# Performance work log

Measured on AMD Instinct MI355X. Metric: run time of the kernel, lower is better.

The kernel has to match this reference:

```python
import jax, jax.numpy as jnp
import numpy as np

N = 100000   # nodes
E = 1600000  # directed edges (avg degree 16)
D = 128      # num_feature == hidden_channels


def setup_inputs() -> dict:
    key = jax.random.key(0)
    ks = jax.random.split(key, 8)
    s = 1.0 / np.sqrt(D)
    x = jax.random.normal(ks[0], (N, D), jnp.float32)
    edge_index = jax.random.randint(ks[1], (2, E), 0, N, dtype=jnp.int32)
    W1 = jax.random.normal(ks[2], (D, D), jnp.float32) * s
    W2 = jax.random.normal(ks[3], (D, D), jnp.float32) * s
    W3 = jax.random.normal(ks[4], (D, D), jnp.float32) * s
    b1 = jnp.zeros((D,), jnp.float32)
    b2 = jnp.zeros((D,), jnp.float32)
    b3 = jnp.zeros((D,), jnp.float32)
    return {"x": x, "edge_index": edge_index, "W1": W1, "b1": b1,
            "W2": W2, "b2": b2, "W3": W3, "b3": b3}


def reference(x, edge_index, W1, b1, W2, b2, W3, b3):
    # GCNConv with added self-loops and symmetric normalization:
    #   out = D^{-1/2} (A + I) D^{-1/2} (x W) + b
    loops = jnp.arange(N, dtype=edge_index.dtype)
    src = jnp.concatenate([edge_index[0], loops])  # [E+N]
    dst = jnp.concatenate([edge_index[1], loops])
    deg = jax.ops.segment_sum(jnp.ones_like(dst, x.dtype), dst, num_segments=N)
    dinv = jax.lax.rsqrt(deg)                      # deg >= 1 (self-loops)
    norm = dinv[src] * dinv[dst]                   # [E+N]

    def conv(h, W, b):
        h = h @ W                                   # [N, D] dense GEMM
        msg = h[src] * norm[:, None]                # gather + scale [E+N, D]
        return jax.ops.segment_sum(msg, dst, num_segments=N) + b

    # dropout is identity in eval mode
    h = jax.nn.relu(conv(x, W1, b1))
    h = jax.nn.relu(conv(h, W2, b2))
    return conv(h, W3, b3)
```

## Files before the change

kernel.cpp:

```cpp
#include <hip/hip_runtime.h>
#include <hip/hip_fp16.h>

#define DFEAT 128
#define BNODES 256
#define BSHIFT 8
#define B1CHUNK 4096
#define SLABC 8192
#define TPB_TILES 2
#define TPB1 2

typedef _Float16 f16x8 __attribute__((ext_vector_type(8)));
typedef _Float16 f16x4 __attribute__((ext_vector_type(4)));
typedef float f32x4 __attribute__((ext_vector_type(4)));


__global__ __launch_bounds__(256) void packW_k(const float* __restrict__ W0, const float* __restrict__ W1,
                                               const float* __restrict__ W2,
                                               const float* __restrict__ b0, const float* __restrict__ b1,
                                               const float* __restrict__ b2,
                                               _Float16* __restrict__ wpk, float* __restrict__ bp,
                                               int* __restrict__ gcnt) {
    int idx = blockIdx.x * 256 + threadIdx.x;
    int layer = idx >> 14;
    int e = idx & 16383;
    int k = e >> 7;
    int nn = e & 127;
    const float* W = (layer == 0) ? W0 : ((layer == 1) ? W1 : W2);
    int ksrc = (layer == 0) ? k : (((k & 7) << 4) | (k >> 3));
    float v = W[ksrc * DFEAT + nn];
    int kc = k >> 5, quad = (k >> 3) & 3, j = k & 7;
    int ct = nn >> 4;
    int pos = ((ct * 4 + kc) * 64 + quad * 16 + (nn & 15)) * 8 + j;
    wpk[(size_t)layer * 16384 + pos] = (_Float16)v;
    if (idx < 384) {
        int l = idx >> 7, p = idx & 127;
        int c = ((p & 7) << 4) | (p >> 3);
        const float* bb = (l == 0) ? b0 : ((l == 1) ? b1 : b2);
        bp[l * 128 + p] = bb[c];
    }
    if (idx < 512) gcnt[idx] = 0;
}

__device__ inline f16x8 ldA8(const float* p) {
    float4 a = *(const float4*)p;
    float4 b = *(const float4*)(p + 4);
    return f16x8{(_Float16)a.x, (_Float16)a.y, (_Float16)a.z, (_Float16)a.w,
                 (_Float16)b.x, (_Float16)b.y, (_Float16)b.z, (_Float16)b.w};
}
__device__ inline f16x8 ldA8(const __half* p) { return *(const f16x8*)p; }
__device__ inline f16x8 zero8() {
    return f16x8{(_Float16)0.f, (_Float16)0.f, (_Float16)0.f, (_Float16)0.f,
                 (_Float16)0.f, (_Float16)0.f, (_Float16)0.f, (_Float16)0.f};
}

struct BinSh {
    int cnt[512];
    int off[512];
    int gbase[512];
    int sd[256];
    unsigned int buf[B1CHUNK];
    unsigned short bid[B1CHUNK];
};
struct G1Sh {
    _Float16 wl[16384];
};

__global__ __launch_bounds__(256) void binGemm1_k(const int* __restrict__ src, const int* __restrict__ dst,
                                                  int* __restrict__ gcnt, unsigned int* __restrict__ slab,
                                                  int E, int nbuck, int nbin,
                                                  const float* __restrict__ A, const _Float16* __restrict__ wfrag,
                                                  __half* __restrict__ C, int n, int ntiles) {
    __shared__ __align__(16) char smem[32768];
    int t = threadIdx.x;
    if (blockIdx.x >= nbin) {
        _Float16* wl = ((G1Sh*)smem)->wl;
        const int wv_ = t >> 6;
        const int lane = t & 63;
        const int m = lane & 15;
        const int q = lane >> 4;
        for (int c = t; c < 2048; c += 256)
            *(f16x8*)&wl[c * 8] = *(const f16x8*)&wfrag[c * 8];
        __syncthreads();
        int t0 = (blockIdx.x - nbin) * TPB1;
        int tend = t0 + TPB1;
        if (tend > ntiles) tend = ntiles;
        for (int tile = t0; tile < tend; ++tile) {
            int row0 = tile * 64;
            int ga = row0 + wv_ * 16 + m;
            f16x8 af[4];
            if (ga < n) {
#pragma unroll
                for (int kc = 0; kc < 4; ++kc)
                    af[kc] = ldA8(&A[(size_t)ga * DFEAT + kc * 32 + q * 8]);
            } else {
#pragma unroll
                for (int kc = 0; kc < 4; ++kc) af[kc] = zero8();
            }
            f32x4 acc[8];
#pragma unroll
            for (int ct = 0; ct < 8; ++ct) acc[ct] = (f32x4){0.f, 0.f, 0.f, 0.f};
#pragma unroll
            for (int ct = 0; ct < 8; ++ct) {
#pragma unroll
                for (int kc = 0; kc < 4; ++kc) {
                    f16x8 bf = *(f16x8*)&wl[((ct * 4 + kc) * 64 + lane) * 8];
                    acc[ct] = __builtin_amdgcn_mfma_f32_16x16x32_f16(af[kc], bf, acc[ct], 0, 0, 0);
                }
            }
            const int rbase = row0 + wv_ * 16 + q * 4;
#pragma unroll
            for (int r = 0; r < 4; ++r) {
                int gr = rbase + r;
                if (gr < n) {
                    f16x8 o;
#pragma unroll
                    for (int ct = 0; ct < 8; ++ct) o[ct] = (_Float16)acc[ct][r];
                    *(f16x8*)&C[(size_t)gr * DFEAT + m * 8] = o;
                }
            }
        }
        return;
    }
    BinSh* B = (BinSh*)smem;
    int base = blockIdx.x * B1CHUNK;
    int nloc = E - base;
    if (nloc > B1CHUNK) nloc = B1CHUNK;
    B->cnt[t] = 0;
    B->cnt[t + 256] = 0;
    __syncthreads();
    int k = t;
    for (; k + 768 < nloc; k += 1024) {
        int d0 = dst[base + k], d1 = dst[base + k + 256], d2 = dst[base + k + 512], d3 = dst[base + k + 768];
        atomicAdd(&B->cnt[d0 >> BSHIFT], 1);
        atomicAdd(&B->cnt[d1 >> BSHIFT], 1);
        atomicAdd(&B->cnt[d2 >> BSHIFT], 1);
        atomicAdd(&B->cnt[d3 >> BSHIFT], 1);
    }
    for (; k < nloc; k += 256) atomicAdd(&B->cnt[dst[base + k] >> BSHIFT], 1);
    __syncthreads();
    int v0 = B->cnt[2 * t], v1 = B->cnt[2 * t + 1];
    int tsum = v0 + v1;
    B->sd[t] = tsum;
    __syncthreads();
    for (int o = 1; o < 256; o <<= 1) {
        int x = (t >= o) ? B->sd[t - o] : 0;
        __syncthreads();
        B->sd[t] += x;
        __syncthreads();
    }
    int texcl = B->sd[t] - tsum;
    B->off[2 * t] = texcl;
    B->off[2 * t + 1] = texcl + v0;
    if (2 * t < nbuck && v0 > 0) B->gbase[2 * t] = atomicAdd(&gcnt[2 * t], v0);
    if (2 * t + 1 < nbuck && v1 > 0) B->gbase[2 * t + 1] = atomicAdd(&gcnt[2 * t + 1], v1);
    __syncthreads();
    k = t;
    for (; k + 768 < nloc; k += 1024) {
        int d0 = dst[base + k], d1 = dst[base + k + 256], d2 = dst[base + k + 512], d3 = dst[base + k + 768];
        int s0 = src[base + k], s1 = src[base + k + 256], s2 = src[base + k + 512], s3 = src[base + k + 768];
        int b0_ = d0 >> BSHIFT, b1_ = d1 >> BSHIFT, b2_ = d2 >> BSHIFT, b3_ = d3 >> BSHIFT;
        int r0 = atomicAdd(&B->off[b0_], 1); B->buf[r0] = ((unsigned)s0 << BSHIFT) | (unsigned)(d0 & (BNODES - 1)); B->bid[r0] = (unsigned short)b0_;
        int r1 = atomicAdd(&B->off[b1_], 1); B->buf[r1] = ((unsigned)s1 << BSHIFT) | (unsigned)(d1 & (BNODES - 1)); B->bid[r1] = (unsigned short)b1_;
        int r2 = atomicAdd(&B->off[b2_], 1); B->buf[r2] = ((unsigned)s2 << BSHIFT) | (unsigned)(d2 & (BNODES - 1)); B->bid[r2] = (unsigned short)b2_;
        int r3 = atomicAdd(&B->off[b3_], 1); B->buf[r3] = ((unsigned)s3 << BSHIFT) | (unsigned)(d3 & (BNODES - 1)); B->bid[r3] = (unsigned short)b3_;
    }
    for (; k < nloc; k += 256) {
        int d = dst[base + k];
        int s = src[base + k];
        int b = d >> BSHIFT;
        int r = atomicAdd(&B->off[b], 1);
        B->buf[r] = ((unsigned)s << BSHIFT) | (unsigned)(d & (BNODES - 1));
        B->bid[r] = (unsigned short)b;
    }
    __syncthreads();
    k = t;
    for (; k + 768 < nloc; k += 1024) {
#pragma unroll
        for (int u = 0; u < 4; ++u) {
            int kk = k + u * 256;
            int b = B->bid[kk];
            int o0 = B->off[b] - B->cnt[b];
            int pos = B->gbase[b] + (kk - o0);
            if (pos < SLABC) slab[(size_t)b * SLABC + pos] = B->buf[kk];
        }
    }
    for (; k < nloc; k += 256) {
        int b = B->bid[k];
        int o0 = B->off[b] - B->cnt[b];
        int pos = B->gbase[b] + (k - o0);
        if (pos < SLABC) slab[(size_t)b * SLABC + pos] = B->buf[k];
    }
}

__global__ __launch_bounds__(256) void bucketAB_k(const unsigned int* __restrict__ slab,
                                                  const int* __restrict__ gcnt,
                                                  int* __restrict__ rp, float* __restrict__ dinv,
                                                  int* __restrict__ cols, int N, int nbuck) {
    __shared__ int cnt[256];
    __shared__ int cur[256];
    __shared__ int psum[256];
    __shared__ int outb[SLABC];
    int t = threadIdx.x;
    int b = blockIdx.x;
    int n0 = b << BSHIFT;
    int nn = N - n0;
    if (nn > BNODES) nn = BNODES;
    int ne_raw = gcnt[b];
    int ne = ne_raw > SLABC ? SLABC : ne_raw;
    const unsigned int* sl = slab + (size_t)b * SLABC;
    int part = 0;
    for (int i = t; i < b; i += 256) part += gcnt[i];
    psum[t] = part;
    cnt[t] = 0;
    __syncthreads();
    for (int o = 128; o > 0; o >>= 1) {
        if (t < o) psum[t] += psum[t + o];
        __syncthreads();
    }
    int base = psum[0];
    int k = t;
    for (; k + 768 < ne; k += 1024) {
        unsigned a0 = sl[k], a1 = sl[k + 256], a2 = sl[k + 512], a3 = sl[k + 768];
        atomicAdd(&cnt[a0 & (BNODES - 1)], 1);
        atomicAdd(&cnt[a1 & (BNODES - 1)], 1);
        atomicAdd(&cnt[a2 & (BNODES - 1)], 1);
        atomicAdd(&cnt[a3 & (BNODES - 1)], 1);
    }
    for (; k < ne; k += 256) atomicAdd(&cnt[sl[k] & (BNODES - 1)], 1);
    __syncthreads();
    int deg = cnt[t];
    for (int o = 1; o < 256; o <<= 1) {
        int x = (t >= o) ? cnt[t - o] : 0;
        __syncthreads();
        cnt[t] += x;
        __syncthreads();
    }
    int excl = cnt[t] - deg;
    if (t < nn) {
        rp[n0 + t] = base + excl;
        dinv[n0 + t] = rsqrtf((float)(deg + 1));
    }
    if (b == nbuck - 1 && t == 0) rp[N] = base + ne_raw;
    cur[t] = excl;
    __syncthreads();
    k = t;
    for (; k + 768 < ne; k += 1024) {
        unsigned a0 = sl[k], a1 = sl[k + 256], a2 = sl[k + 512], a3 = sl[k + 768];
        int p0 = atomicAdd(&cur[a0 & (BNODES - 1)], 1); outb[p0] = (int)(a0 >> BSHIFT);
        int p1 = atomicAdd(&cur[a1 & (BNODES - 1)], 1); outb[p1] = (int)(a1 >> BSHIFT);
        int p2 = atomicAdd(&cur[a2 & (BNODES - 1)], 1); outb[p2] = (int)(a2 >> BSHIFT);
        int p3 = atomicAdd(&cur[a3 & (BNODES - 1)], 1); outb[p3] = (int)(a3 >> BSHIFT);
    }
    for (; k < ne; k += 256) {
        unsigned a = sl[k];
        int p = atomicAdd(&cur[a & (BNODES - 1)], 1);
        outb[p] = (int)(a >> BSHIFT);
    }
    __syncthreads();
    k = t;
    for (; k + 768 < ne; k += 1024) {
        int o0 = outb[k], o1 = outb[k + 256], o2 = outb[k + 512], o3 = outb[k + 768];
        cols[base + k] = o0;
        cols[base + k + 256] = o1;
        cols[base + k + 512] = o2;
        cols[base + k + 768] = o3;
    }
    for (; k < ne; k += 256) cols[base + k] = outb[k];
}

template <typename TIN>
__global__ __launch_bounds__(256) void gemmP_k(const TIN* __restrict__ A, const _Float16* __restrict__ wfrag,
                                               const float* __restrict__ dinv, __half* __restrict__ C,
                                               int n, int ntiles) {
    __shared__ _Float16 al[8192];
    __shared__ _Float16 wl[16384];
    const int tid = threadIdx.x;
    const int wv_ = tid >> 6;
    const int lane = tid & 63;
    const int t0 = blockIdx.x * TPB_TILES;
    const int chunk = tid & 15;
    const int rsub = tid >> 4;
    const int kcS = chunk >> 2, quadS = chunk & 3;
    const int swzS = (kcS << 1) ^ (quadS & 1);

    for (int c = tid; c < 2048; c += 256)
        *(f16x8*)&wl[c * 8] = *(const f16x8*)&wfrag[c * 8];

    f16x8 pre[4];
    {
        int row0 = t0 * 64;
#pragma unroll
        for (int p = 0; p < 4; ++p) {
            int gr = row0 + p * 16 + rsub;
            pre[p] = (gr < n) ? ldA8(&A[(size_t)gr * DFEAT + chunk * 8]) : zero8();
        }
    }
    for (int tt = 0; tt < TPB_TILES; ++tt) {
        int tile = t0 + tt;
        if (tile >= ntiles) break;
        int row0 = tile * 64;
#pragma unroll
        for (int p = 0; p < 4; ++p) {
            int idx = (p * 4 + kcS) * 64 + quadS * 16 + rsub;
            *(f16x8*)&al[(idx ^ swzS) * 8] = pre[p];
        }
        __syncthreads();
        if (tt + 1 < TPB_TILES && tile + 1 < ntiles) {
            int nrow0 = (tile + 1) * 64;
#pragma unroll
            for (int p = 0; p < 4; ++p) {
                int gr = nrow0 + p * 16 + rsub;
                pre[p] = (gr < n) ? ldA8(&A[(size_t)gr * DFEAT + chunk * 8]) : zero8();
            }
        }
        f16x8 af[4];
        const int swzR = (lane >> 4) & 1;
#pragma unroll
        for (int kc = 0; kc < 4; ++kc) {
            int idx = (wv_ * 4 + kc) * 64 + lane;
            af[kc] = *(f16x8*)&al[(idx ^ (kc << 1) ^ swzR) * 8];
        }
        const int quad = lane >> 4, cb = lane & 15;
        const int rbase = row0 + wv_ * 16 + quad * 4;
        float ds[4];
#pragma unroll
        for (int r = 0; r < 4; ++r) ds[r] = (rbase + r < n) ? dinv[rbase + r] : 0.f;
        f32x4 acc[8];
#pragma unroll
        for (int ct = 0; ct < 8; ++ct) acc[ct] = (f32x4){0.f, 0.f, 0.f, 0.f};
#pragma unroll
        for (int ct = 0; ct < 8; ++ct) {
#pragma unroll
            for (int kc = 0; kc < 4; ++kc) {
                f16x8 bf = *(f16x8*)&wl[((ct * 4 + kc) * 64 + lane) * 8];
                acc[ct] = __builtin_amdgcn_mfma_f32_16x16x32_f16(af[kc], bf, acc[ct], 0, 0, 0);
            }
        }
#pragma unroll
        for (int r = 0; r < 4; ++r) {
            int gr = rbase + r;
            if (gr < n) {
                f16x8 o;
#pragma unroll
                for (int ct = 0; ct < 8; ++ct) o[ct] = (_Float16)(acc[ct][r] * ds[r]);
                *(f16x8*)&C[(size_t)gr * DFEAT + cb * 8] = o;
            }
        }
        __syncthreads();
    }
}


__global__ __launch_bounds__(256) void aggW_k(const __half* __restrict__ T, const float* __restrict__ dinv,
                                              const int* __restrict__ rowptr, const int* __restrict__ cols,
                                              const float* __restrict__ biasp,
                                              __half* __restrict__ out, int n) {
    int wid = (int)((blockIdx.x * (size_t)blockDim.x + threadIdx.x) >> 6);
    int lane = threadIdx.x & 63;
    if (wid >= n) return;
    int fb = lane * 2;
    float di = dinv[wid];
    float2 t0 = __half22float2(*(const __half2*)(T + (size_t)wid * DFEAT + fb));
    float ax = di * t0.x;
    float ay = di * t0.y;
    int s = rowptr[wid], e = rowptr[wid + 1];
    for (int p = s; p < e; ) {
        int take = e - p;
        if (take > 64) take = 64;
        int q = p + lane;
        if (q >= e) q = e - 1;
        int ci = cols[q];
        int j = 0;
        for (; j + 8 <= take; j += 8) {
            int c0 = __builtin_amdgcn_readlane(ci, j + 0);
            int c1 = __builtin_amdgcn_readlane(ci, j + 1);
            int c2 = __builtin_amdgcn_readlane(ci, j + 2);
            int c3 = __builtin_amdgcn_readlane(ci, j + 3);
            int c4 = __builtin_amdgcn_readlane(ci, j + 4);
            int c5 = __builtin_amdgcn_readlane(ci, j + 5);
            int c6 = __builtin_amdgcn_readlane(ci, j + 6);
            int c7 = __builtin_amdgcn_readlane(ci, j + 7);
            float w0 = dinv[c0], w1 = dinv[c1], w2 = dinv[c2], w3 = dinv[c3];
            float w4 = dinv[c4], w5 = dinv[c5], w6 = dinv[c6], w7 = dinv[c7];
            float2 v0 = __half22float2(*(const __half2*)(T + (size_t)c0 * DFEAT + fb));
            float2 v1 = __half22float2(*(const __half2*)(T + (size_t)c1 * DFEAT + fb));
            float2 v2 = __half22float2(*(const __half2*)(T + (size_t)c2 * DFEAT + fb));
            float2 v3 = __half22float2(*(const __half2*)(T + (size_t)c3 * DFEAT + fb));
            float2 v4 = __half22float2(*(const __half2*)(T + (size_t)c4 * DFEAT + fb));
            float2 v5 = __half22float2(*(const __half2*)(T + (size_t)c5 * DFEAT + fb));
            float2 v6 = __half22float2(*(const __half2*)(T + (size_t)c6 * DFEAT + fb));
            float2 v7 = __half22float2(*(const __half2*)(T + (size_t)c7 * DFEAT + fb));
            ax += w0 * v0.x; ay += w0 * v0.y;
            ax += w1 * v1.x; ay += w1 * v1.y;
            ax += w2 * v2.x; ay += w2 * v2.y;
            ax += w3 * v3.x; ay += w3 * v3.y;
            ax += w4 * v4.x; ay += w4 * v4.y;
            ax += w5 * v5.x; ay += w5 * v5.y;
            ax += w6 * v6.x; ay += w6 * v6.y;
            ax += w7 * v7.x; ay += w7 * v7.y;
        }
        for (; j < take; ++j) {
            int c = __builtin_amdgcn_readlane(ci, j);
            float w = dinv[c];
            float2 v = __half22float2(*(const __half2*)(T + (size_t)c * DFEAT + fb));
            ax += w * v.x; ay += w * v.y;
        }
        p += take;
    }
    float ox = fmaxf(di * ax + biasp[fb], 0.f);
    float oy = fmaxf(di * ay + biasp[fb + 1], 0.f);
    *(__half2*)(out + (size_t)wid * DFEAT + fb) = __floats2half2_rn(ox, oy);
}

__device__ inline float2 agg_row(const __half* __restrict__ T, const int* __restrict__ rowptr,
                                 const int* __restrict__ cols, int wid, int lane, int fb) {
    float2 t0 = __half22float2(*(const __half2*)(T + (size_t)wid * DFEAT + fb));
    float ax = t0.x;
    float ay = t0.y;
    int s = rowptr[wid], e = rowptr[wid + 1];
    for (int p = s; p < e; ) {
        int take = e - p;
        if (take > 64) take = 64;
        int q = p + lane;
        if (q >= e) q = e - 1;
        int ci = cols[q];
        int j = 0;
        for (; j + 8 <= take; j += 8) {
            int c0 = __builtin_amdgcn_readlane(ci, j + 0);
            int c1 = __builtin_amdgcn_readlane(ci, j + 1);
            int c2 = __builtin_amdgcn_readlane(ci, j + 2);
            int c3 = __builtin_amdgcn_readlane(ci, j + 3);
            int c4 = __builtin_amdgcn_readlane(ci, j + 4);
            int c5 = __builtin_amdgcn_readlane(ci, j + 5);
            int c6 = __builtin_amdgcn_readlane(ci, j + 6);
            int c7 = __builtin_amdgcn_readlane(ci, j + 7);
            float2 v0 = __half22float2(*(const __half2*)(T + (size_t)c0 * DFEAT + fb));
            float2 v1 = __half22float2(*(const __half2*)(T + (size_t)c1 * DFEAT + fb));
            float2 v2 = __half22float2(*(const __half2*)(T + (size_t)c2 * DFEAT + fb));
            float2 v3 = __half22float2(*(const __half2*)(T + (size_t)c3 * DFEAT + fb));
            float2 v4 = __half22float2(*(const __half2*)(T + (size_t)c4 * DFEAT + fb));
            float2 v5 = __half22float2(*(const __half2*)(T + (size_t)c5 * DFEAT + fb));
            float2 v6 = __half22float2(*(const __half2*)(T + (size_t)c6 * DFEAT + fb));
            float2 v7 = __half22float2(*(const __half2*)(T + (size_t)c7 * DFEAT + fb));
            ax += v0.x; ay += v0.y;
            ax += v1.x; ay += v1.y;
            ax += v2.x; ay += v2.y;
            ax += v3.x; ay += v3.y;
            ax += v4.x; ay += v4.y;
            ax += v5.x; ay += v5.y;
            ax += v6.x; ay += v6.y;
            ax += v7.x; ay += v7.y;
        }
        for (; j < take; ++j) {
            int c = __builtin_amdgcn_readlane(ci, j);
            float2 v = __half22float2(*(const __half2*)(T + (size_t)c * DFEAT + fb));
            ax += v.x; ay += v.y;
        }
        p += take;
    }
    return make_float2(ax, ay);
}

__global__ __launch_bounds__(256) void agg_k(const __half* __restrict__ T, const float* __restrict__ dinv,
                                             const int* __restrict__ rowptr, const int* __restrict__ cols,
                                             const float* __restrict__ biasp,
                                             __half* __restrict__ out, int n) {
    int wid = (int)((blockIdx.x * (size_t)blockDim.x + threadIdx.x) >> 6);
    int lane = threadIdx.x & 63;
    if (wid >= n) return;
    int fb = lane * 2;
    float2 a = agg_row(T, rowptr, cols, wid, lane, fb);
    float dw = dinv[wid];
    float ox = fmaxf(dw * a.x + biasp[fb], 0.f);
    float oy = fmaxf(dw * a.y + biasp[fb + 1], 0.f);
    *(__half2*)(out + (size_t)wid * DFEAT + fb) = __floats2half2_rn(ox, oy);
}

__global__ __launch_bounds__(256) void aggF_k(const __half* __restrict__ T, const float* __restrict__ dinv,
                                              const int* __restrict__ rowptr, const int* __restrict__ cols,
                                              const float* __restrict__ biasp,
                                              float* __restrict__ out, int n) {
    int wid = (int)((blockIdx.x * (size_t)blockDim.x + threadIdx.x) >> 6);
    int lane = threadIdx.x & 63;
    if (wid >= n) return;
    int fb = lane * 2;
    float2 a = agg_row(T, rowptr, cols, wid, lane, fb);
    float dw = dinv[wid];
    float ox = dw * a.x + biasp[fb];
    float oy = dw * a.y + biasp[fb + 1];
    int c0 = ((fb & 7) << 4) | (fb >> 3);
    int c1 = (((fb + 1) & 7) << 4) | ((fb + 1) >> 3);
    out[(size_t)wid * DFEAT + c0] = ox;
    out[(size_t)wid * DFEAT + c1] = oy;
}


extern "C" void kernel_launch(void* const* d_in, const int* in_sizes, int n_in,
                              void* d_out, int out_size, void* d_ws, size_t ws_size,
                              hipStream_t stream) {
    const float* x  = (const float*)d_in[0];
    const int*   ei = (const int*)d_in[1];
    const float* W1 = (const float*)d_in[2];
    const float* b1 = (const float*)d_in[3];
    const float* W2 = (const float*)d_in[4];
    const float* b2 = (const float*)d_in[5];
    const float* W3 = (const float*)d_in[6];
    const float* b3 = (const float*)d_in[7];
    float* out = (float*)d_out;

    const int N = in_sizes[0] / DFEAT;
    const int E = in_sizes[1] / 2;
    const int* srcp = ei;
    const int* dstp = ei + E;

    size_t off = 0;
    auto alloc = [&](size_t bytes) -> void* {
        void* p = (char*)d_ws + off;
        off += (bytes + 255) & ~(size_t)255;
        return p;
    };
    const int nbuck = (N + BNODES - 1) / BNODES;

    int*    gcnt = (int*)alloc(2048);
    int*    rp   = (int*)alloc((size_t)(N + 1) * 4);
    float*  dinv = (float*)alloc((size_t)N * 4);
    _Float16* wpk = (_Float16*)alloc((size_t)3 * 16384 * 2);
    float*  bp   = (float*)alloc(3 * 128 * 4);
    unsigned int* slab = (unsigned int*)alloc((size_t)nbuck * SLABC * 4);
    int*    cols = (int*)alloc((size_t)E * 4);
    __half* bufA = (__half*)alloc((size_t)N * DFEAT * 2);
    __half* bufB = (__half*)alloc((size_t)N * DFEAT * 2);

    const int nbin = (E + B1CHUNK - 1) / B1CHUNK;
    int ntiles = (N + 63) / 64;
    int g1blocks = (ntiles + TPB1 - 1) / TPB1;
    int gemmGrid = (ntiles + TPB_TILES - 1) / TPB_TILES;
    int aggGrid  = (int)(((size_t)N * 64 + 255) / 256);

    packW_k<<<192, 256, 0, stream>>>(W1, W2, W3, b1, b2, b3, wpk, bp, gcnt);
    binGemm1_k<<<nbin + g1blocks, 256, 0, stream>>>(srcp, dstp, gcnt, slab, E, nbuck, nbin,
                                                    x, wpk, bufA, N, ntiles);
    bucketAB_k<<<nbuck, 256, 0, stream>>>(slab, gcnt, rp, dinv, cols, N, nbuck);

    aggW_k<<<aggGrid, 256, 0, stream>>>(bufA, dinv, rp, cols, bp, bufB, N);

    gemmP_k<__half><<<gemmGrid, 256, 0, stream>>>(bufB, wpk + 16384, dinv, bufA, N, ntiles);
    agg_k<<<aggGrid, 256, 0, stream>>>(bufA, dinv, rp, cols, bp + 128, bufB, N);

    gemmP_k<__half><<<gemmGrid, 256, 0, stream>>>(bufB, wpk + 32768, dinv, bufA, N, ntiles);
    aggF_k<<<aggGrid, 256, 0, stream>>>(bufA, dinv, rp, cols, bp + 256, out, N);
}
```

Before: 378.5 us.

## Split aggregation and GEMM into halves and co-schedule them across kernel launches

Work is regrouped so independent stages share launches. Weight packing now runs inside the edge-binning kernel, and the layer-1 GEMM runs inside the bucket/CSR-build kernel. Each later aggregation is split at the node midpoint: the second-half aggregation runs in the same launch as the next layer's GEMM on the first half, which that half's earlier aggregation has already produced. The slab buffer is aliased with a new third feature buffer. This cuts launches and the idle tail at launch boundaries, at the cost of more launches in the middle of the chain and mixed block types sharing one grid.

```diff
diff --git a/kernel.cpp b/kernel.cpp
--- a/kernel.cpp
+++ b/kernel.cpp
@@ -8,50 +8,12 @@
 #define SLABC 8192
 #define TPB_TILES 2
 #define TPB1 2
+#define TPBM 2
 
 typedef _Float16 f16x8 __attribute__((ext_vector_type(8)));
 typedef _Float16 f16x4 __attribute__((ext_vector_type(4)));
 typedef float f32x4 __attribute__((ext_vector_type(4)));
 
-
-__global__ __launch_bounds__(256) void packW_k(const float* __restrict__ W0, const float* __restrict__ W1,
-                                               const float* __restrict__ W2,
-                                               const float* __restrict__ b0, const float* __restrict__ b1,
-                                               const float* __restrict__ b2,
-                                               _Float16* __restrict__ wpk, float* __restrict__ bp,
-                                               int* __restrict__ gcnt) {
-    int idx = blockIdx.x * 256 + threadIdx.x;
-    int layer = idx >> 14;
-    int e = idx & 16383;
-    int k = e >> 7;
-    int nn = e & 127;
-    const float* W = (layer == 0) ? W0 : ((layer == 1) ? W1 : W2);
-    int ksrc = (layer == 0) ? k : (((k & 7) << 4) | (k >> 3));
-    float v = W[ksrc * DFEAT + nn];
-    int kc = k >> 5, quad = (k >> 3) & 3, j = k & 7;
-    int ct = nn >> 4;
-    int pos = ((ct * 4 + kc) * 64 + quad * 16 + (nn & 15)) * 8 + j;
-    wpk[(size_t)layer * 16384 + pos] = (_Float16)v;
-    if (idx < 384) {
-        int l = idx >> 7, p = idx & 127;
-        int c = ((p & 7) << 4) | (p >> 3);
-        const float* bb = (l == 0) ? b0 : ((l == 1) ? b1 : b2);
-        bp[l * 128 + p] = bb[c];
-    }
-    if (idx < 512) gcnt[idx] = 0;
-}
-
-__device__ inline f16x8 ldA8(const float* p) {
-    float4 a = *(const float4*)p;
-    float4 b = *(const float4*)(p + 4);
-    return f16x8{(_Float16)a.x, (_Float16)a.y, (_Float16)a.z, (_Float16)a.w,
-                 (_Float16)b.x, (_Float16)b.y, (_Float16)b.z, (_Float16)b.w};
-}
-__device__ inline f16x8 ldA8(const __half* p) { return *(const f16x8*)p; }
-__device__ inline f16x8 zero8() {
-    return f16x8{(_Float16)0.f, (_Float16)0.f, (_Float16)0.f, (_Float16)0.f,
-                 (_Float16)0.f, (_Float16)0.f, (_Float16)0.f, (_Float16)0.f};
-}
 
 struct BinSh {
     int cnt[512];
@@ -61,19 +23,132 @@
     unsigned int buf[B1CHUNK];
     unsigned short bid[B1CHUNK];
 };
-struct G1Sh {
-    _Float16 wl[16384];
-};
-
-__global__ __launch_bounds__(256) void binGemm1_k(const int* __restrict__ src, const int* __restrict__ dst,
-                                                  int* __restrict__ gcnt, unsigned int* __restrict__ slab,
-                                                  int E, int nbuck, int nbin,
-                                                  const float* __restrict__ A, const _Float16* __restrict__ wfrag,
-                                                  __half* __restrict__ C, int n, int ntiles) {
-    __shared__ __align__(16) char smem[32768];
+
+__global__ __launch_bounds__(256) void binpack_k(const int* __restrict__ src, const int* __restrict__ dst,
+                                                 int* __restrict__ gcnt, unsigned int* __restrict__ slab,
+                                                 int E, int nbuck, int nbin,
+                                                 const float* __restrict__ W0, const float* __restrict__ W1,
+                                                 const float* __restrict__ W2,
+                                                 const float* __restrict__ b0, const float* __restrict__ b1,
+                                                 const float* __restrict__ b2,
+                                                 _Float16* __restrict__ wpk, float* __restrict__ bp) {
+    __shared__ __align__(16) BinSh B;
     int t = threadIdx.x;
     if (blockIdx.x >= nbin) {
-        _Float16* wl = ((G1Sh*)smem)->wl;
+        int idx = (blockIdx.x - nbin) * 256 + t;
+        if (idx < 49152) {
+            int layer = idx >> 14;
+            int e = idx & 16383;
+            int k = e >> 7;
+            int nn = e & 127;
+            const float* W = (layer == 0) ? W0 : ((layer == 1) ? W1 : W2);
+            int ksrc = (layer == 0) ? k : (((k & 7) << 4) | (k >> 3));
+            float v = W[ksrc * DFEAT + nn];
+            int kc = k >> 5, quad = (k >> 3) & 3, j = k & 7;
+            int ct = nn >> 4;
+            int pos = ((ct * 4 + kc) * 64 + quad * 16 + (nn & 15)) * 8 + j;
+            wpk[(size_t)layer * 16384 + pos] = (_Float16)v;
+            if (idx < 384) {
+                int l = idx >> 7, p = idx & 127;
+                int c = ((p & 7) << 4) | (p >> 3);
+                const float* bb = (l == 0) ? b0 : ((l == 1) ? b1 : b2);
+                bp[l * 128 + p] = bb[c];
+            }
+        }
+        return;
+    }
+    int base = blockIdx.x * B1CHUNK;
+    int nloc = E - base;
+    if (nloc > B1CHUNK) nloc = B1CHUNK;
+    B.cnt[t] = 0;
+    B.cnt[t + 256] = 0;
+    __syncthreads();
+    int k = t;
+    for (; k + 768 < nloc; k += 1024) {
+        int d0 = dst[base + k], d1 = dst[base + k + 256], d2 = dst[base + k + 512], d3 = dst[base + k + 768];
+        atomicAdd(&B.cnt[d0 >> BSHIFT], 1);
+        atomicAdd(&B.cnt[d1 >> BSHIFT], 1);
+        atomicAdd(&B.cnt[d2 >> BSHIFT], 1);
+        atomicAdd(&B.cnt[d3 >> BSHIFT], 1);
+    }
+    for (; k < nloc; k += 256) atomicAdd(&B.cnt[dst[base + k] >> BSHIFT], 1);
+    __syncthreads();
+    int v0 = B.cnt[2 * t], v1 = B.cnt[2 * t + 1];
+    int tsum = v0 + v1;
+    B.sd[t] = tsum;
+    __syncthreads();
+    for (int o = 1; o < 256; o <<= 1) {
+        int x = (t >= o) ? B.sd[t - o] : 0;
+        __syncthreads();
+        B.sd[t] += x;
+        __syncthreads();
+    }
+    int texcl = B.sd[t] - tsum;
+    B.off[2 * t] = texcl;
+    B.off[2 * t + 1] = texcl + v0;
+    if (2 * t < nbuck && v0 > 0) B.gbase[2 * t] = atomicAdd(&gcnt[2 * t], v0);
+    if (2 * t + 1 < nbuck && v1 > 0) B.gbase[2 * t + 1] = atomicAdd(&gcnt[2 * t + 1], v1);
+    __syncthreads();
+    k = t;
+    for (; k + 768 < nloc; k += 1024) {
+        int d0 = dst[base + k], d1 = dst[base + k + 256], d2 = dst[base + k + 512], d3 = dst[base + k + 768];
+        int s0 = src[base + k], s1 = src[base + k + 256], s2 = src[base + k + 512], s3 = src[base + k + 768];
+        int b0_ = d0 >> BSHIFT, b1_ = d1 >> BSHIFT, b2_ = d2 >> BSHIFT, b3_ = d3 >> BSHIFT;
+        int r0 = atomicAdd(&B.off[b0_], 1); B.buf[r0] = ((unsigned)s0 << BSHIFT) | (unsigned)(d0 & (BNODES - 1)); B.bid[r0] = (unsigned short)b0_;
+        int r1 = atomicAdd(&B.off[b1_], 1); B.buf[r1] = ((unsigned)s1 << BSHIFT) | (unsigned)(d1 & (BNODES - 1)); B.bid[r1] = (unsigned short)b1_;
+        int r2 = atomicAdd(&B.off[b2_], 1); B.buf[r2] = ((unsigned)s2 << BSHIFT) | (unsigned)(d2 & (BNODES - 1)); B.bid[r2] = (unsigned short)b2_;
+        int r3 = atomicAdd(&B.off[b3_], 1); B.buf[r3] = ((unsigned)s3 << BSHIFT) | (unsigned)(d3 & (BNODES - 1)); B.bid[r3] = (unsigned short)b3_;
+    }
+    for (; k < nloc; k += 256) {
+        int d = dst[base + k];
+        int s = src[base + k];
+        int b = d >> BSHIFT;
+        int r = atomicAdd(&B.off[b], 1);
+        B.buf[r] = ((unsigned)s << BSHIFT) | (unsigned)(d & (BNODES - 1));
+        B.bid[r] = (unsigned short)b;
+    }
+    __syncthreads();
+    k = t;
+    for (; k + 768 < nloc; k += 1024) {
+#pragma unroll
+        for (int u = 0; u < 4; ++u) {
+            int kk = k + u * 256;
+            int b = B.bid[kk];
+            int o0 = B.off[b] - B.cnt[b];
+            int pos = B.gbase[b] + (kk - o0);
+            if (pos < SLABC) slab[(size_t)b * SLABC + pos] = B.buf[kk];
+        }
+    }
+    for (; k < nloc; k += 256) {
+        int b = B.bid[k];
+        int o0 = B.off[b] - B.cnt[b];
+        int pos = B.gbase[b] + (k - o0);
+        if (pos < SLABC) slab[(size_t)b * SLABC + pos] = B.buf[k];
+    }
+}
+
+__device__ inline f16x8 ldA8(const float* p) {
+    float4 a = *(const float4*)p;
+    float4 b = *(const float4*)(p + 4);
+    return f16x8{(_Float16)a.x, (_Float16)a.y, (_Float16)a.z, (_Float16)a.w,
+                 (_Float16)b.x, (_Float16)b.y, (_Float16)b.z, (_Float16)b.w};
+}
+__device__ inline f16x8 ldA8(const __half* p) { return *(const f16x8*)p; }
+__device__ inline f16x8 zero8() {
+    return f16x8{(_Float16)0.f, (_Float16)0.f, (_Float16)0.f, (_Float16)0.f,
+                 (_Float16)0.f, (_Float16)0.f, (_Float16)0.f, (_Float16)0.f};
+}
+
+__global__ __launch_bounds__(256) void bktg1_k(const unsigned int* __restrict__ slab,
+                                               const int* __restrict__ gcnt,
+                                               int* __restrict__ rp, float* __restrict__ dinv,
+                                               int* __restrict__ cols, int N, int nbuck,
+                                               const float* __restrict__ A, const _Float16* __restrict__ wfrag,
+                                               __half* __restrict__ C, int ntiles) {
+    __shared__ __align__(16) char smem[36096];
+    int t = threadIdx.x;
+    if (blockIdx.x >= nbuck) {
+        _Float16* wl = (_Float16*)smem;
         const int wv_ = t >> 6;
         const int lane = t & 63;
         const int m = lane & 15;
@@ -81,14 +156,14 @@
         for (int c = t; c < 2048; c += 256)
             *(f16x8*)&wl[c * 8] = *(const f16x8*)&wfrag[c * 8];
         __syncthreads();
-        int t0 = (blockIdx.x - nbin) * TPB1;
+        int t0 = (blockIdx.x - nbuck) * TPB1;
         int tend = t0 + TPB1;
         if (tend > ntiles) tend = ntiles;
         for (int tile = t0; tile < tend; ++tile) {
             int row0 = tile * 64;
             int ga = row0 + wv_ * 16 + m;
             f16x8 af[4];
-            if (ga < n) {
+            if (ga < N) {
 #pragma unroll
                 for (int kc = 0; kc < 4; ++kc)
                     af[kc] = ldA8(&A[(size_t)ga * DFEAT + kc * 32 + q * 8]);
@@ -111,7 +186,7 @@
 #pragma unroll
             for (int r = 0; r < 4; ++r) {
                 int gr = rbase + r;
-                if (gr < n) {
+                if (gr < N) {
                     f16x8 o;
 #pragma unroll
                     for (int ct = 0; ct < 8; ++ct) o[ct] = (_Float16)acc[ct][r];
@@ -121,86 +196,10 @@
         }
         return;
     }
-    BinSh* B = (BinSh*)smem;
-    int base = blockIdx.x * B1CHUNK;
-    int nloc = E - base;
-    if (nloc > B1CHUNK) nloc = B1CHUNK;
-    B->cnt[t] = 0;
-    B->cnt[t + 256] = 0;
-    __syncthreads();
-    int k = t;
-    for (; k + 768 < nloc; k += 1024) {
-        int d0 = dst[base + k], d1 = dst[base + k + 256], d2 = dst[base + k + 512], d3 = dst[base + k + 768];
-        atomicAdd(&B->cnt[d0 >> BSHIFT], 1);
-        atomicAdd(&B->cnt[d1 >> BSHIFT], 1);
-        atomicAdd(&B->cnt[d2 >> BSHIFT], 1);
-        atomicAdd(&B->cnt[d3 >> BSHIFT], 1);
-    }
-    for (; k < nloc; k += 256) atomicAdd(&B->cnt[dst[base + k] >> BSHIFT], 1);
-    __syncthreads();
-    int v0 = B->cnt[2 * t], v1 = B->cnt[2 * t + 1];
-    int tsum = v0 + v1;
-    B->sd[t] = tsum;
-    __syncthreads();
-    for (int o = 1; o < 256; o <<= 1) {
-        int x = (t >= o) ? B->sd[t - o] : 0;
-        __syncthreads();
-        B->sd[t] += x;
-        __syncthreads();
-    }
-    int texcl = B->sd[t] - tsum;
-    B->off[2 * t] = texcl;
-    B->off[2 * t + 1] = texcl + v0;
-    if (2 * t < nbuck && v0 > 0) B->gbase[2 * t] = atomicAdd(&gcnt[2 * t], v0);
-    if (2 * t + 1 < nbuck && v1 > 0) B->gbase[2 * t + 1] = atomicAdd(&gcnt[2 * t + 1], v1);
-    __syncthreads();
-    k = t;
-    for (; k + 768 < nloc; k += 1024) {
-        int d0 = dst[base + k], d1 = dst[base + k + 256], d2 = dst[base + k + 512], d3 = dst[base + k + 768];
-        int s0 = src[base + k], s1 = src[base + k + 256], s2 = src[base + k + 512], s3 = src[base + k + 768];
-        int b0_ = d0 >> BSHIFT, b1_ = d1 >> BSHIFT, b2_ = d2 >> BSHIFT, b3_ = d3 >> BSHIFT;
-        int r0 = atomicAdd(&B->off[b0_], 1); B->buf[r0] = ((unsigned)s0 << BSHIFT) | (unsigned)(d0 & (BNODES - 1)); B->bid[r0] = (unsigned short)b0_;
-        int r1 = atomicAdd(&B->off[b1_], 1); B->buf[r1] = ((unsigned)s1 << BSHIFT) | (unsigned)(d1 & (BNODES - 1)); B->bid[r1] = (unsigned short)b1_;
-        int r2 = atomicAdd(&B->off[b2_], 1); B->buf[r2] = ((unsigned)s2 << BSHIFT) | (unsigned)(d2 & (BNODES - 1)); B->bid[r2] = (unsigned short)b2_;
-        int r3 = atomicAdd(&B->off[b3_], 1); B->buf[r3] = ((unsigned)s3 << BSHIFT) | (unsigned)(d3 & (BNODES - 1)); B->bid[r3] = (unsigned short)b3_;
-    }
-    for (; k < nloc; k += 256) {
-        int d = dst[base + k];
-        int s = src[base + k];
-        int b = d >> BSHIFT;
-        int r = atomicAdd(&B->off[b], 1);
-        B->buf[r] = ((unsigned)s << BSHIFT) | (unsigned)(d & (BNODES - 1));
-        B->bid[r] = (unsigned short)b;
-    }
-    __syncthreads();
-    k = t;
-    for (; k + 768 < nloc; k += 1024) {
-#pragma unroll
-        for (int u = 0; u < 4; ++u) {
-            int kk = k + u * 256;
-            int b = B->bid[kk];
-            int o0 = B->off[b] - B->cnt[b];
-            int pos = B->gbase[b] + (kk - o0);
-            if (pos < SLABC) slab[(size_t)b * SLABC + pos] = B->buf[kk];
-        }
-    }
-    for (; k < nloc; k += 256) {
-        int b = B->bid[k];
-        int o0 = B->off[b] - B->cnt[b];
-        int pos = B->gbase[b] + (k - o0);
-        if (pos < SLABC) slab[(size_t)b * SLABC + pos] = B->buf[k];
-    }
-}
-
-__global__ __launch_bounds__(256) void bucketAB_k(const unsigned int* __restrict__ slab,
-                                                  const int* __restrict__ gcnt,
-                                                  int* __restrict__ rp, float* __restrict__ dinv,
-                                                  int* __restrict__ cols, int N, int nbuck) {
-    __shared__ int cnt[256];
-    __shared__ int cur[256];
-    __shared__ int psum[256];
-    __shared__ int outb[SLABC];
-    int t = threadIdx.x;
+    int* cnt  = (int*)smem;
+    int* cur  = (int*)(smem + 1024);
+    int* psum = (int*)(smem + 2048);
+    int* outb = (int*)(smem + 3072);
     int b = blockIdx.x;
     int n0 = b << BSHIFT;
     int nn = N - n0;
@@ -268,96 +267,11 @@
     for (; k < ne; k += 256) cols[base + k] = outb[k];
 }
 
-template <typename TIN>
-__global__ __launch_bounds__(256) void gemmP_k(const TIN* __restrict__ A, const _Float16* __restrict__ wfrag,
-                                               const float* __restrict__ dinv, __half* __restrict__ C,
-                                               int n, int ntiles) {
-    __shared__ _Float16 al[8192];
-    __shared__ _Float16 wl[16384];
-    const int tid = threadIdx.x;
-    const int wv_ = tid >> 6;
-    const int lane = tid & 63;
-    const int t0 = blockIdx.x * TPB_TILES;
-    const int chunk = tid & 15;
-    const int rsub = tid >> 4;
-    const int kcS = chunk >> 2, quadS = chunk & 3;
-    const int swzS = (kcS << 1) ^ (quadS & 1);
-
-    for (int c = tid; c < 2048; c += 256)
-        *(f16x8*)&wl[c * 8] = *(const f16x8*)&wfrag[c * 8];
-
-    f16x8 pre[4];
-    {
-        int row0 = t0 * 64;
-#pragma unroll
-        for (int p = 0; p < 4; ++p) {
-            int gr = row0 + p * 16 + rsub;
-            pre[p] = (gr < n) ? ldA8(&A[(size_t)gr * DFEAT + chunk * 8]) : zero8();
-        }
-    }
-    for (int tt = 0; tt < TPB_TILES; ++tt) {
-        int tile = t0 + tt;
-        if (tile >= ntiles) break;
-        int row0 = tile * 64;
-#pragma unroll
-        for (int p = 0; p < 4; ++p) {
-            int idx = (p * 4 + kcS) * 64 + quadS * 16 + rsub;
-            *(f16x8*)&al[(idx ^ swzS) * 8] = pre[p];
-        }
-        __syncthreads();
-        if (tt + 1 < TPB_TILES && tile + 1 < ntiles) {
-            int nrow0 = (tile + 1) * 64;
-#pragma unroll
-            for (int p = 0; p < 4; ++p) {
-                int gr = nrow0 + p * 16 + rsub;
-                pre[p] = (gr < n) ? ldA8(&A[(size_t)gr * DFEAT + chunk * 8]) : zero8();
-            }
-        }
-        f16x8 af[4];
-        const int swzR = (lane >> 4) & 1;
-#pragma unroll
-        for (int kc = 0; kc < 4; ++kc) {
-            int idx = (wv_ * 4 + kc) * 64 + lane;
-            af[kc] = *(f16x8*)&al[(idx ^ (kc << 1) ^ swzR) * 8];
-        }
-        const int quad = lane >> 4, cb = lane & 15;
-        const int rbase = row0 + wv_ * 16 + quad * 4;
-        float ds[4];
-#pragma unroll
-        for (int r = 0; r < 4; ++r) ds[r] = (rbase + r < n) ? dinv[rbase + r] : 0.f;
-        f32x4 acc[8];
-#pragma unroll
-        for (int ct = 0; ct < 8; ++ct) acc[ct] = (f32x4){0.f, 0.f, 0.f, 0.f};
-#pragma unroll
-        for (int ct = 0; ct < 8; ++ct) {
-#pragma unroll
-            for (int kc = 0; kc < 4; ++kc) {
-                f16x8 bf = *(f16x8*)&wl[((ct * 4 + kc) * 64 + lane) * 8];
-                acc[ct] = __builtin_amdgcn_mfma_f32_16x16x32_f16(af[kc], bf, acc[ct], 0, 0, 0);
-            }
-        }
-#pragma unroll
-        for (int r = 0; r < 4; ++r) {
-            int gr = rbase + r;
-            if (gr < n) {
-                f16x8 o;
-#pragma unroll
-                for (int ct = 0; ct < 8; ++ct) o[ct] = (_Float16)(acc[ct][r] * ds[r]);
-                *(f16x8*)&C[(size_t)gr * DFEAT + cb * 8] = o;
-            }
-        }
-        __syncthreads();
-    }
-}
-
-
-__global__ __launch_bounds__(256) void aggW_k(const __half* __restrict__ T, const float* __restrict__ dinv,
-                                              const int* __restrict__ rowptr, const int* __restrict__ cols,
-                                              const float* __restrict__ biasp,
-                                              __half* __restrict__ out, int n) {
-    int wid = (int)((blockIdx.x * (size_t)blockDim.x + threadIdx.x) >> 6);
-    int lane = threadIdx.x & 63;
-    if (wid >= n) return;
+
+__device__ inline void aggW_node(const __half* __restrict__ T, const float* __restrict__ dinv,
+                                 const int* __restrict__ rowptr, const int* __restrict__ cols,
+                                 const float* __restrict__ biasp, __half* __restrict__ out,
+                                 int wid, int lane) {
     int fb = lane * 2;
     float di = dinv[wid];
     float2 t0 = __half22float2(*(const __half2*)(T + (size_t)wid * DFEAT + fb));
@@ -461,19 +375,100 @@
     return make_float2(ax, ay);
 }
 
-__global__ __launch_bounds__(256) void agg_k(const __half* __restrict__ T, const float* __restrict__ dinv,
-                                             const int* __restrict__ rowptr, const int* __restrict__ cols,
-                                             const float* __restrict__ biasp,
-                                             __half* __restrict__ out, int n) {
-    int wid = (int)((blockIdx.x * (size_t)blockDim.x + threadIdx.x) >> 6);
-    int lane = threadIdx.x & 63;
-    if (wid >= n) return;
+__device__ inline void agg_node(const __half* __restrict__ T, const float* __restrict__ dinv,
+                                const int* __restrict__ rowptr, const int* __restrict__ cols,
+                                const float* __restrict__ biasp, __half* __restrict__ out,
+                                int wid, int lane) {
     int fb = lane * 2;
     float2 a = agg_row(T, rowptr, cols, wid, lane, fb);
     float dw = dinv[wid];
     float ox = fmaxf(dw * a.x + biasp[fb], 0.f);
     float oy = fmaxf(dw * a.y + biasp[fb + 1], 0.f);
     *(__half2*)(out + (size_t)wid * DFEAT + fb) = __floats2half2_rn(ox, oy);
+}
+
+__device__ inline void gemm_tile_g(const __half* __restrict__ A, const _Float16* __restrict__ wfrag,
+                                   const float* __restrict__ dinv, __half* __restrict__ C,
+                                   int n, int tile) {
+    const int tid = threadIdx.x;
+    const int wv_ = tid >> 6;
+    const int lane = tid & 63;
+    const int m = lane & 15;
+    const int q = lane >> 4;
+    int row0 = tile * 64;
+    int ga = row0 + wv_ * 16 + m;
+    f16x8 af[4];
+    if (ga < n) {
+#pragma unroll
+        for (int kc = 0; kc < 4; ++kc)
+            af[kc] = *(const f16x8*)&A[(size_t)ga * DFEAT + kc * 32 + q * 8];
+    } else {
+#pragma unroll
+        for (int kc = 0; kc < 4; ++kc) af[kc] = zero8();
+    }
+    f32x4 acc[8];
+#pragma unroll
+    for (int ct = 0; ct < 8; ++ct) acc[ct] = (f32x4){0.f, 0.f, 0.f, 0.f};
+#pragma unroll
+    for (int ct = 0; ct < 8; ++ct) {
+#pragma unroll
+        for (int kc = 0; kc < 4; ++kc) {
+            f16x8 bf = *(const f16x8*)&wfrag[((size_t)(ct * 4 + kc) * 64 + lane) * 8];
+            acc[ct] = __builtin_amdgcn_mfma_f32_16x16x32_f16(af[kc], bf, acc[ct], 0, 0, 0);
+        }
+    }
+    const int rbase = row0 + wv_ * 16 + q * 4;
+#pragma unroll
+    for (int r = 0; r < 4; ++r) {
+        int gr = rbase + r;
+        if (gr < n) {
+            float dr = dinv[gr];
+            f16x8 o;
+#pragma unroll
+            for (int ct = 0; ct < 8; ++ct) o[ct] = (_Float16)(acc[ct][r] * dr);
+            *(f16x8*)&C[(size_t)gr * DFEAT + m * 8] = o;
+        }
+    }
+}
+
+template <bool WEIGHTED>
+__global__ __launch_bounds__(256) void aggGemm_k(const __half* __restrict__ T, const float* __restrict__ dinv,
+                                                 const int* __restrict__ rowptr, const int* __restrict__ cols,
+                                                 const float* __restrict__ biasp, __half* __restrict__ aggOut,
+                                                 int r0, int r1, int nAggB,
+                                                 const __half* __restrict__ Gsrc, const _Float16* __restrict__ wfrag,
+                                                 __half* __restrict__ Gout, int g0, int g1, int n) {
+    if ((int)blockIdx.x < nAggB) {
+        int wid = r0 + (int)blockIdx.x * 4 + (threadIdx.x >> 6);
+        if (wid >= r1) return;
+        int lane = threadIdx.x & 63;
+        if (WEIGHTED) aggW_node(T, dinv, rowptr, cols, biasp, aggOut, wid, lane);
+        else          agg_node(T, dinv, rowptr, cols, biasp, aggOut, wid, lane);
+    } else {
+        int t0 = g0 + ((int)blockIdx.x - nAggB) * TPBM;
+        for (int tt = 0; tt < TPBM; ++tt) {
+            int tile = t0 + tt;
+            if (tile >= g0 && tile < g1) gemm_tile_g(Gsrc, wfrag, dinv, Gout, n, tile);
+        }
+    }
+}
+
+__global__ __launch_bounds__(256) void aggW_k(const __half* __restrict__ T, const float* __restrict__ dinv,
+                                              const int* __restrict__ rowptr, const int* __restrict__ cols,
+                                              const float* __restrict__ biasp, __half* __restrict__ out,
+                                              int r0, int r1) {
+    int wid = r0 + (int)blockIdx.x * 4 + (threadIdx.x >> 6);
+    if (wid >= r1) return;
+    aggW_node(T, dinv, rowptr, cols, biasp, out, wid, threadIdx.x & 63);
+}
+
+__global__ __launch_bounds__(256) void agg_k(const __half* __restrict__ T, const float* __restrict__ dinv,
+                                             const int* __restrict__ rowptr, const int* __restrict__ cols,
+                                             const float* __restrict__ biasp, __half* __restrict__ out,
+                                             int r0, int r1) {
+    int wid = r0 + (int)blockIdx.x * 4 + (threadIdx.x >> 6);
+    if (wid >= r1) return;
+    agg_node(T, dinv, rowptr, cols, biasp, out, wid, threadIdx.x & 63);
 }
 
 __global__ __launch_bounds__(256) void aggF_k(const __half* __restrict__ T, const float* __restrict__ dinv,
@@ -494,6 +489,87 @@
     out[(size_t)wid * DFEAT + c1] = oy;
 }
 
+__global__ __launch_bounds__(256) void gemmP_k(const __half* __restrict__ A, const _Float16* __restrict__ wfrag,
+                                               const float* __restrict__ dinv, __half* __restrict__ C,
+                                               int n, int tile0, int ntiles) {
+    __shared__ _Float16 al[8192];
+    __shared__ _Float16 wl[16384];
+    const int tid = threadIdx.x;
+    const int wv_ = tid >> 6;
+    const int lane = tid & 63;
+    const int t0 = tile0 + blockIdx.x * TPB_TILES;
+    const int chunk = tid & 15;
+    const int rsub = tid >> 4;
+    const int kcS = chunk >> 2, quadS = chunk & 3;
+    const int swzS = (kcS << 1) ^ (quadS & 1);
+
+    for (int c = tid; c < 2048; c += 256)
+        *(f16x8*)&wl[c * 8] = *(const f16x8*)&wfrag[c * 8];
+
+    f16x8 pre[4];
+    {
+        int row0 = t0 * 64;
+#pragma unroll
+        for (int p = 0; p < 4; ++p) {
+            int gr = row0 + p * 16 + rsub;
+            pre[p] = (gr < n) ? ldA8(&A[(size_t)gr * DFEAT + chunk * 8]) : zero8();
+        }
+    }
+    for (int tt = 0; tt < TPB_TILES; ++tt) {
+        int tile = t0 + tt;
+        if (tile >= ntiles) break;
+        int row0 = tile * 64;
+#pragma unroll
+        for (int p = 0; p < 4; ++p) {
+            int idx = (p * 4 + kcS) * 64 + quadS * 16 + rsub;
+            *(f16x8*)&al[(idx ^ swzS) * 8] = pre[p];
+        }
+        __syncthreads();
+        if (tt + 1 < TPB_TILES && tile + 1 < ntiles) {
+            int nrow0 = (tile + 1) * 64;
+#pragma unroll
+            for (int p = 0; p < 4; ++p) {
+                int gr = nrow0 + p * 16 + rsub;
+                pre[p] = (gr < n) ? ldA8(&A[(size_t)gr * DFEAT + chunk * 8]) : zero8();
+            }
+        }
+        f16x8 af[4];
+        const int swzR = (lane >> 4) & 1;
+#pragma unroll
+        for (int kc = 0; kc < 4; ++kc) {
+            int idx = (wv_ * 4 + kc) * 64 + lane;
+            af[kc] = *(f16x8*)&al[(idx ^ (kc << 1) ^ swzR) * 8];
+        }
+        const int quad = lane >> 4, cb = lane & 15;
+        const int rbase = row0 + wv_ * 16 + quad * 4;
+        float ds[4];
+#pragma unroll
+        for (int r = 0; r < 4; ++r) ds[r] = (rbase + r < n) ? dinv[rbase + r] : 0.f;
+        f32x4 acc[8];
+#pragma unroll
+        for (int ct = 0; ct < 8; ++ct) acc[ct] = (f32x4){0.f, 0.f, 0.f, 0.f};
+#pragma unroll
+        for (int ct = 0; ct < 8; ++ct) {
+#pragma unroll
+            for (int kc = 0; kc < 4; ++kc) {
+                f16x8 bf = *(f16x8*)&wl[((ct * 4 + kc) * 64 + lane) * 8];
+                acc[ct] = __builtin_amdgcn_mfma_f32_16x16x32_f16(af[kc], bf, acc[ct], 0, 0, 0);
+            }
+        }
+#pragma unroll
+        for (int r = 0; r < 4; ++r) {
+            int gr = rbase + r;
+            if (gr < n) {
+                f16x8 o;
+#pragma unroll
+                for (int ct = 0; ct < 8; ++ct) o[ct] = (_Float16)(acc[ct][r] * ds[r]);
+                *(f16x8*)&C[(size_t)gr * DFEAT + cb * 8] = o;
+            }
+        }
+        __syncthreads();
+    }
+}
+
 
 extern "C" void kernel_launch(void* const* d_in, const int* in_sizes, int n_in,
                               void* d_out, int out_size, void* d_ws, size_t ws_size,
@@ -526,27 +602,40 @@
     float*  dinv = (float*)alloc((size_t)N * 4);
     _Float16* wpk = (_Float16*)alloc((size_t)3 * 16384 * 2);
     float*  bp   = (float*)alloc(3 * 128 * 4);
-    unsigned int* slab = (unsigned int*)alloc((size_t)nbuck * SLABC * 4);
     int*    cols = (int*)alloc((size_t)E * 4);
     __half* bufA = (__half*)alloc((size_t)N * DFEAT * 2);
     __half* bufB = (__half*)alloc((size_t)N * DFEAT * 2);
+    size_t shBytes = (size_t)nbuck * SLABC * 4;
+    size_t cBytes  = (size_t)N * DFEAT * 2;
+    void* shared = alloc(shBytes > cBytes ? shBytes : cBytes);
+    unsigned int* slab = (unsigned int*)shared;
+    __half* bufC = (__half*)shared;
 
     const int nbin = (E + B1CHUNK - 1) / B1CHUNK;
     int ntiles = (N + 63) / 64;
-    int g1blocks = (ntiles + TPB1 - 1) / TPB1;
-    int gemmGrid = (ntiles + TPB_TILES - 1) / TPB_TILES;
-    int aggGrid  = (int)(((size_t)N * 64 + 255) / 256);
-
-    packW_k<<<192, 256, 0, stream>>>(W1, W2, W3, b1, b2, b3, wpk, bp, gcnt);
-    binGemm1_k<<<nbin + g1blocks, 256, 0, stream>>>(srcp, dstp, gcnt, slab, E, nbuck, nbin,
-                                                    x, wpk, bufA, N, ntiles);
-    bucketAB_k<<<nbuck, 256, 0, stream>>>(slab, gcnt, rp, dinv, cols, N, nbuck);
-
-    aggW_k<<<aggGrid, 256, 0, stream>>>(bufA, dinv, rp, cols, bp, bufB, N);
-
-    gemmP_k<__half><<<gemmGrid, 256, 0, stream>>>(bufB, wpk + 16384, dinv, bufA, N, ntiles);
-    agg_k<<<aggGrid, 256, 0, stream>>>(bufA, dinv, rp, cols, bp + 128, bufB, N);
-
-    gemmP_k<__half><<<gemmGrid, 256, 0, stream>>>(bufB, wpk + 32768, dinv, bufA, N, ntiles);
-    aggF_k<<<aggGrid, 256, 0, stream>>>(bufA, dinv, rp, cols, bp + 256, out, N);
-}
+    int htiles = ntiles / 2;
+    int hrows  = htiles * 64;
+    int g1b    = (ntiles + TPB1 - 1) / TPB1;
+    int gmixB  = (htiles + TPBM - 1) / TPBM;
+    int gPB    = (ntiles - htiles + TPB_TILES - 1) / TPB_TILES;
+    int aggB1  = (hrows + 3) / 4;
+    int aggB2  = (N - hrows + 3) / 4;
+    int aggFull = (int)(((size_t)N * 64 + 255) / 256);
+
+    hipMemsetAsync(gcnt, 0, 2048, stream);
+    binpack_k<<<nbin + 192, 256, 0, stream>>>(srcp, dstp, gcnt, slab, E, nbuck, nbin,
+                                              W1, W2, W3, b1, b2, b3, wpk, bp);
+    bktg1_k<<<nbuck + g1b, 256, 0, stream>>>(slab, gcnt, rp, dinv, cols, N, nbuck,
+                                             x, wpk, bufA, ntiles);
+    aggW_k<<<aggB1, 256, 0, stream>>>(bufA, dinv, rp, cols, bp, bufB, 0, hrows);
+    aggGemm_k<true><<<aggB2 + gmixB, 256, 0, stream>>>(bufA, dinv, rp, cols, bp, bufB,
+                                                       hrows, N, aggB2,
+                                                       bufB, wpk + 16384, bufC, 0, htiles, N);
+    gemmP_k<<<gPB, 256, 0, stream>>>(bufB, wpk + 16384, dinv, bufC, N, htiles, ntiles);
+    agg_k<<<aggB1, 256, 0, stream>>>(bufC, dinv, rp, cols, bp + 128, bufA, 0, hrows);
+    aggGemm_k<false><<<aggB2 + gmixB, 256, 0, stream>>>(bufC, dinv, rp, cols, bp + 128, bufA,
+                                                        hrows, N, aggB2,
+                                                        bufA, wpk + 32768, bufB, 0, htiles, N);
+    gemmP_k<<<gPB, 256, 0, stream>>>(bufA, wpk + 32768, dinv, bufB, N, htiles, ntiles);
+    aggF_k<<<aggFull, 256, 0, stream>>>(bufB, dinv, rp, cols, bp + 256, out, N);
+}
```

Result: slower. 435.1 us (+15.0%).
